# Optimization experiments

Measured on AMD Instinct MI355X. Metric: run time of the kernel, lower is better.

Reference implementation:

```python
import jax, jax.numpy as jnp
import numpy as np

NEG_SLOPE = 0.01  # torch nn.LeakyReLU default


def setup_inputs() -> dict:
    key = jax.random.key(0)
    k1, k2, k3 = jax.random.split(key, 3)
    B, H, D, L = 4, 8, 64, 2048
    q = jax.random.normal(k1, (B, H, D, L), dtype=jnp.float32)
    k = jax.random.normal(k2, (B, H, D, L), dtype=jnp.float32)
    v = jax.random.normal(k3, (B, H, D, L), dtype=jnp.float32)
    return {"q": q, "k": k, "v": v}


def reference(q, k, v):
    # q, k, v: [B, H, D, L] (note: feature dim BEFORE length, as in the torch module)
    d_tensor = q.shape[2]
    scale = 1.0 / np.sqrt(d_tensor).astype(np.float32)
    # scores = LeakyReLU(q^T k / sqrt(d)) : [B, H, Lq, Lk]
    scores = jnp.einsum('bhdq,bhdk->bhqk', q, k) * scale
    scores = jax.nn.leaky_relu(scores, negative_slope=NEG_SLOPE)
    psi = jax.nn.softmax(scores, axis=-1)
    # out = (psi @ v^T)^T : [B, H, D, Lq]
    out = jnp.einsum('bhqk,bhdk->bhdq', psi, v)
    return out
```

## Files before the change

kernel.cpp:

```cpp
#include <hip/hip_runtime.h>
#include <math.h>

#define DD 64
#define LL 2048
#define TQ 128
#define TK 64
#define NTHREADS 512
#define QSCALE 0.18033688011112042f

typedef __bf16 bf16_t;
typedef __bf16 bf16x8 __attribute__((ext_vector_type(8)));
typedef float f32x16 __attribute__((ext_vector_type(16)));

struct __align__(16) SMemA {
  bf16_t Qs[TQ][72];
  bf16_t Ks[TK][72];
  bf16_t Vs[DD][72];
};
union __align__(16) SMemU {
  SMemA a;
  float Oe[TQ][65];
};

__global__ __launch_bounds__(NTHREADS, 4)
void attn_flash_bf16(const float* __restrict__ q, const float* __restrict__ k,
                     const float* __restrict__ v, float* __restrict__ out) {
  __shared__ SMemU sm;
  __shared__ float rs1[TQ];
  const int tid  = threadIdx.x;
  const int w    = tid >> 6;
  const int lane = tid & 63;
  const int l31  = lane & 31;
  const int hh   = lane >> 5;
  const int strip = w & 3;
  const int half  = w >> 2;
  const int wbase = strip * 32;
  const int lkh   = half * 32;
  const int head = blockIdx.y;
  const int q0   = blockIdx.x * TQ;
  const size_t hoff = (size_t)head * DD * LL;
  const float* qp = q + hoff;
  const float* kp = k + hoff;
  const float* vp = v + hoff;

  {
    int lq  = tid & 127;
    int d0q = (tid >> 7) * 16;
    const float* src = qp + q0 + lq;
    for (int g = 0; g < 2; ++g) {
      bf16x8 pk;
      for (int j = 0; j < 8; ++j)
        pk[j] = (bf16_t)(src[(size_t)(d0q + g * 8 + j) * LL] * QSCALE);
      *(bf16x8*)&sm.a.Qs[lq][d0q + g * 8] = pk;
    }
  }

  const int klk = tid & 63;
  const int kd0 = (tid >> 6) * 8;
  const int vd  = tid >> 3;
  const int vc8 = (tid & 7) * 8;

  float  kreg[8];
  float4 vreg[2];
  {
    const float* ks = kp + klk;
    for (int j = 0; j < 8; ++j) kreg[j] = ks[(size_t)(kd0 + j) * LL];
    vreg[0] = *(const float4*)(vp + (size_t)vd * LL + vc8);
    vreg[1] = *(const float4*)(vp + (size_t)vd * LL + vc8 + 4);
  }

  __syncthreads();
  bf16x8 bq[4];
  for (int kk = 0; kk < 4; ++kk)
    bq[kk] = *(const bf16x8*)&sm.a.Qs[wbase + l31][kk * 16 + 8 * hh];

  f32x16 oacc[2];
  for (int dt = 0; dt < 2; ++dt)
    for (int r = 0; r < 16; ++r) oacc[dt][r] = 0.f;
  float rsum = 0.f;

  for (int t = 0; t < LL / TK; ++t) {
    __syncthreads();
    {
      bf16x8 pk;
      for (int j = 0; j < 8; ++j) pk[j] = (bf16_t)kreg[j];
      *(bf16x8*)&sm.a.Ks[klk][kd0] = pk;
      bf16x8 pv;
      pv[0] = (bf16_t)vreg[0].x; pv[1] = (bf16_t)vreg[0].y;
      pv[2] = (bf16_t)vreg[0].z; pv[3] = (bf16_t)vreg[0].w;
      pv[4] = (bf16_t)vreg[1].x; pv[5] = (bf16_t)vreg[1].y;
      pv[6] = (bf16_t)vreg[1].z; pv[7] = (bf16_t)vreg[1].w;
      *(bf16x8*)&sm.a.Vs[vd][vc8] = pv;
    }
    __syncthreads();

    if (t + 1 < LL / TK) {
      const int lk0n = (t + 1) * TK;
      const float* ks = kp + lk0n + klk;
      for (int j = 0; j < 8; ++j) kreg[j] = ks[(size_t)(kd0 + j) * LL];
      vreg[0] = *(const float4*)(vp + (size_t)vd * LL + lk0n + vc8);
      vreg[1] = *(const float4*)(vp + (size_t)vd * LL + lk0n + vc8 + 4);
    }

    f32x16 st;
    for (int r = 0; r < 16; ++r) st[r] = 0.f;
    for (int kk = 0; kk < 4; ++kk) {
      bf16x8 ak = *(const bf16x8*)&sm.a.Ks[lkh + l31][kk * 16 + 8 * hh];
      st = __builtin_amdgcn_mfma_f32_32x32x16_bf16(ak, bq[kk], st, 0, 0, 0);
    }

    unsigned pb[8];
    for (int r = 0; r < 16; ++r) {
      float s = st[r];
      s = fmaxf(s, 0.01f * s);
      float p = __builtin_amdgcn_exp2f(s);
      rsum += p;
      st[r] = p;
    }
    for (int qq = 0; qq < 8; ++qq) {
      union { bf16_t b[2]; unsigned u; } pk;
      pk.b[0] = (bf16_t)st[2 * qq];
      pk.b[1] = (bf16_t)st[2 * qq + 1];
      pb[qq] = pk.u;
    }

    for (int kk2 = 0; kk2 < 2; ++kk2) {
      unsigned l0 = pb[4 * kk2 + 0], l1 = pb[4 * kk2 + 1];
      unsigned l2 = pb[4 * kk2 + 2], l3 = pb[4 * kk2 + 3];
      unsigned s0 = hh ? l0 : l2;
      unsigned s1 = hh ? l1 : l3;
      unsigned f0 = (unsigned)__shfl_xor((int)s0, 32);
      unsigned f1 = (unsigned)__shfl_xor((int)s1, 32);
      union { unsigned u[4]; bf16x8 v; } ap;
      ap.u[0] = hh ? f0 : l0;
      ap.u[1] = hh ? f1 : l1;
      ap.u[2] = hh ? l2 : f0;
      ap.u[3] = hh ? l3 : f1;
      const int lkb = lkh + kk2 * 16 + 8 * hh;
      for (int dt = 0; dt < 2; ++dt) {
        bf16x8 bv = *(const bf16x8*)&sm.a.Vs[dt * 32 + l31][lkb];
        oacc[dt] = __builtin_amdgcn_mfma_f32_32x32x16_bf16(ap.v, bv, oacc[dt], 0, 0, 0);
      }
    }
  }

  float rtot = rsum + __shfl_xor(rsum, 32);
  __syncthreads();
  if (half == 1) {
    rs1[wbase + l31] = rtot;
    for (int r = 0; r < 16; ++r) {
      int row = (r & 3) + 8 * (r >> 2) + 4 * hh;
      for (int dt = 0; dt < 2; ++dt)
        sm.Oe[wbase + row][dt * 32 + l31] = oacc[dt][r];
    }
  }
  __syncthreads();
  if (half == 0) {
    float tot = rtot + rs1[wbase + l31];
    rs1[wbase + l31] = 1.0f / tot;
    float inv[16];
    for (int r = 0; r < 16; ++r) {
      int row = (r & 3) + 8 * (r >> 2) + 4 * hh;
      inv[r] = rs1[wbase + row];
    }
    for (int r = 0; r < 16; ++r) {
      int row = (r & 3) + 8 * (r >> 2) + 4 * hh;
      for (int dt = 0; dt < 2; ++dt) {
        int col = dt * 32 + l31;
        sm.Oe[wbase + row][col] = (oacc[dt][r] + sm.Oe[wbase + row][col]) * inv[r];
      }
    }
  }
  __syncthreads();
  float* op = out + hoff + q0;
  for (int i = 0; i < 16; ++i) {
    int idx = tid + NTHREADS * i;
    int d   = idx >> 7;
    int lq  = idx & 127;
    op[(size_t)d * LL + lq] = sm.Oe[lq][d];
  }
}

extern "C" void kernel_launch(void* const* d_in, const int* in_sizes, int n_in,
                              void* d_out, int out_size, void* d_ws, size_t ws_size,
                              hipStream_t stream) {
  const float* q = (const float*)d_in[0];
  const float* k = (const float*)d_in[1];
  const float* v = (const float*)d_in[2];
  float* out = (float*)d_out;
  dim3 grid(LL / TQ, 32);
  attn_flash_bf16<<<grid, NTHREADS, 0, stream>>>(q, k, v, out);
}
```

Baseline: 145.7 us.

## Double block threads to 1024, widen K tile to 128, drop register prefetch

Doubles the workgroup to 16 waves. Each strip of 32 query rows is now split four ways across the key dimension, with a key tile of 128, and the epilogue reduces four partial outputs through two shared buffers. The register-staged prefetch of the next K/V tile is removed, so global loads now happen directly before the barrier. Q fragments are reloaded from LDS inside the loop instead of being held in registers, trading register pressure for extra LDS reads. The launch bound of 1024 threads with 8 blocks per CU is a hint the hardware cannot meet, and occupancy is likely limited by registers and LDS.

```diff
diff --git a/kernel.cpp b/kernel.cpp
--- a/kernel.cpp
+++ b/kernel.cpp
@@ -4,8 +4,9 @@
 #define DD 64
 #define LL 2048
 #define TQ 128
-#define TK 64
-#define NTHREADS 512
+#define TK 128
+#define NTILES (LL / TK)
+#define NTHREADS 1024
 #define QSCALE 0.18033688011112042f
 
 typedef __bf16 bf16_t;
@@ -15,27 +16,28 @@
 struct __align__(16) SMemA {
   bf16_t Qs[TQ][72];
   bf16_t Ks[TK][72];
-  bf16_t Vs[DD][72];
+  bf16_t Vs[DD][136];
 };
-union __align__(16) SMemU {
-  SMemA a;
-  float Oe[TQ][65];
+struct __align__(16) SMemE {
+  float Oe1[TQ][65];
+  float Oe2[TQ][65];
 };
+union __align__(16) SMemU { SMemA a; SMemE e; };
 
-__global__ __launch_bounds__(NTHREADS, 4)
+__global__ __launch_bounds__(NTHREADS, 8)
 void attn_flash_bf16(const float* __restrict__ q, const float* __restrict__ k,
                      const float* __restrict__ v, float* __restrict__ out) {
   __shared__ SMemU sm;
-  __shared__ float rs1[TQ];
+  __shared__ float rsA[TQ], rsB[TQ];
   const int tid  = threadIdx.x;
   const int w    = tid >> 6;
   const int lane = tid & 63;
   const int l31  = lane & 31;
   const int hh   = lane >> 5;
   const int strip = w & 3;
-  const int half  = w >> 2;
+  const int quart = w >> 2;
   const int wbase = strip * 32;
-  const int lkh   = half * 32;
+  const int lkh   = quart * 32;
   const int head = blockIdx.y;
   const int q0   = blockIdx.x * TQ;
   const size_t hoff = (size_t)head * DD * LL;
@@ -44,69 +46,54 @@
   const float* vp = v + hoff;
 
   {
-    int lq  = tid & 127;
-    int d0q = (tid >> 7) * 16;
+    int lq = tid & 127;
+    int d0 = (tid >> 7) * 8;
     const float* src = qp + q0 + lq;
-    for (int g = 0; g < 2; ++g) {
-      bf16x8 pk;
-      for (int j = 0; j < 8; ++j)
-        pk[j] = (bf16_t)(src[(size_t)(d0q + g * 8 + j) * LL] * QSCALE);
-      *(bf16x8*)&sm.a.Qs[lq][d0q + g * 8] = pk;
-    }
+    bf16x8 pk;
+    for (int j = 0; j < 8; ++j)
+      pk[j] = (bf16_t)(src[(size_t)(d0 + j) * LL] * QSCALE);
+    *(bf16x8*)&sm.a.Qs[lq][d0] = pk;
   }
 
-  const int klk = tid & 63;
-  const int kd0 = (tid >> 6) * 8;
-  const int vd  = tid >> 3;
-  const int vc8 = (tid & 7) * 8;
-
-  float  kreg[8];
-  float4 vreg[2];
-  {
-    const float* ks = kp + klk;
-    for (int j = 0; j < 8; ++j) kreg[j] = ks[(size_t)(kd0 + j) * LL];
-    vreg[0] = *(const float4*)(vp + (size_t)vd * LL + vc8);
-    vreg[1] = *(const float4*)(vp + (size_t)vd * LL + vc8 + 4);
-  }
-
-  __syncthreads();
-  bf16x8 bq[4];
-  for (int kk = 0; kk < 4; ++kk)
-    bq[kk] = *(const bf16x8*)&sm.a.Qs[wbase + l31][kk * 16 + 8 * hh];
+  const int klk = tid & 127;
+  const int kd0 = (tid >> 7) * 8;
+  const int vd  = tid >> 4;
+  const int vc8 = (tid & 15) * 8;
 
   f32x16 oacc[2];
   for (int dt = 0; dt < 2; ++dt)
     for (int r = 0; r < 16; ++r) oacc[dt][r] = 0.f;
   float rsum = 0.f;
 
-  for (int t = 0; t < LL / TK; ++t) {
+  for (int t = 0; t < NTILES; ++t) {
+    const int lk0 = t * TK;
     __syncthreads();
     {
+      const float* src = kp + lk0 + klk;
       bf16x8 pk;
-      for (int j = 0; j < 8; ++j) pk[j] = (bf16_t)kreg[j];
+      for (int j = 0; j < 8; ++j)
+        pk[j] = (bf16_t)src[(size_t)(kd0 + j) * LL];
       *(bf16x8*)&sm.a.Ks[klk][kd0] = pk;
+    }
+    {
+      const float* src = vp + (size_t)vd * LL + lk0 + vc8;
+      float4 a0 = *(const float4*)src;
+      float4 a1 = *(const float4*)(src + 4);
       bf16x8 pv;
-      pv[0] = (bf16_t)vreg[0].x; pv[1] = (bf16_t)vreg[0].y;
-      pv[2] = (bf16_t)vreg[0].z; pv[3] = (bf16_t)vreg[0].w;
-      pv[4] = (bf16_t)vreg[1].x; pv[5] = (bf16_t)vreg[1].y;
-      pv[6] = (bf16_t)vreg[1].z; pv[7] = (bf16_t)vreg[1].w;
+      pv[0] = (bf16_t)a0.x; pv[1] = (bf16_t)a0.y;
+      pv[2] = (bf16_t)a0.z; pv[3] = (bf16_t)a0.w;
+      pv[4] = (bf16_t)a1.x; pv[5] = (bf16_t)a1.y;
+      pv[6] = (bf16_t)a1.z; pv[7] = (bf16_t)a1.w;
       *(bf16x8*)&sm.a.Vs[vd][vc8] = pv;
     }
     __syncthreads();
-
-    if (t + 1 < LL / TK) {
-      const int lk0n = (t + 1) * TK;
-      const float* ks = kp + lk0n + klk;
-      for (int j = 0; j < 8; ++j) kreg[j] = ks[(size_t)(kd0 + j) * LL];
-      vreg[0] = *(const float4*)(vp + (size_t)vd * LL + lk0n + vc8);
-      vreg[1] = *(const float4*)(vp + (size_t)vd * LL + lk0n + vc8 + 4);
-    }
 
     f32x16 st;
     for (int r = 0; r < 16; ++r) st[r] = 0.f;
     for (int kk = 0; kk < 4; ++kk) {
       bf16x8 ak = *(const bf16x8*)&sm.a.Ks[lkh + l31][kk * 16 + 8 * hh];
-      st = __builtin_amdgcn_mfma_f32_32x32x16_bf16(ak, bq[kk], st, 0, 0, 0);
+      bf16x8 bq = *(const bf16x8*)&sm.a.Qs[wbase + l31][kk * 16 + 8 * hh];
+      st = __builtin_amdgcn_mfma_f32_32x32x16_bf16(ak, bq, st, 0, 0, 0);
     }
 
     unsigned pb[8];
@@ -146,38 +133,46 @@
 
   float rtot = rsum + __shfl_xor(rsum, 32);
   __syncthreads();
-  if (half == 1) {
-    rs1[wbase + l31] = rtot;
+  if (quart == 0) {
+    rsA[wbase + l31] = rtot;
     for (int r = 0; r < 16; ++r) {
       int row = (r & 3) + 8 * (r >> 2) + 4 * hh;
       for (int dt = 0; dt < 2; ++dt)
-        sm.Oe[wbase + row][dt * 32 + l31] = oacc[dt][r];
+        sm.e.Oe1[wbase + row][dt * 32 + l31] = oacc[dt][r];
+    }
+  } else if (quart == 2) {
+    rsB[wbase + l31] = rtot;
+    for (int r = 0; r < 16; ++r) {
+      int row = (r & 3) + 8 * (r >> 2) + 4 * hh;
+      for (int dt = 0; dt < 2; ++dt)
+        sm.e.Oe2[wbase + row][dt * 32 + l31] = oacc[dt][r];
     }
   }
   __syncthreads();
-  if (half == 0) {
-    float tot = rtot + rs1[wbase + l31];
-    rs1[wbase + l31] = 1.0f / tot;
-    float inv[16];
+  if (quart == 1) {
+    rsA[wbase + l31] += rtot;
     for (int r = 0; r < 16; ++r) {
       int row = (r & 3) + 8 * (r >> 2) + 4 * hh;
-      inv[r] = rs1[wbase + row];
+      for (int dt = 0; dt < 2; ++dt)
+        sm.e.Oe1[wbase + row][dt * 32 + l31] += oacc[dt][r];
     }
+  } else if (quart == 3) {
+    rsB[wbase + l31] += rtot;
     for (int r = 0; r < 16; ++r) {
       int row = (r & 3) + 8 * (r >> 2) + 4 * hh;
-      for (int dt = 0; dt < 2; ++dt) {
-        int col = dt * 32 + l31;
-        sm.Oe[wbase + row][col] = (oacc[dt][r] + sm.Oe[wbase + row][col]) * inv[r];
-      }
+      for (int dt = 0; dt < 2; ++dt)
+        sm.e.Oe2[wbase + row][dt * 32 + l31] += oacc[dt][r];
     }
   }
   __syncthreads();
+  if (tid < TQ) rsA[tid] = 1.0f / (rsA[tid] + rsB[tid]);
+  __syncthreads();
   float* op = out + hoff + q0;
-  for (int i = 0; i < 16; ++i) {
+  for (int i = 0; i < 8; ++i) {
     int idx = tid + NTHREADS * i;
     int d   = idx >> 7;
     int lq  = idx & 127;
-    op[(size_t)d * LL + lq] = sm.Oe[lq][d];
+    op[(size_t)d * LL + lq] = (sm.e.Oe1[lq][d] + sm.e.Oe2[lq][d]) * rsA[lq];
   }
 }
 
```

Measured after the change: 506.0 us. 3.47x slower.

## Pre-convert Q/K/V to bf16 (transposed Q/K) in workspace before attention

Applied to the files above, without the earlier changes.

Adds pre-pass kernels that convert Q and K to bf16 and transpose them to [L, D] layout, with the softmax scale folded into Q, and convert V to bf16 in place. The attention kernel then reads half as many bytes per K/V tile, with contiguous 16-byte loads instead of strided scalar float loads, and no longer converts inside the inner loop. K and V are each re-read by 16 query blocks, so this lowers repeated global traffic. In exchange it adds three extra launches and a full write/read of the bf16 copies. The old kernel is kept as a fallback when the workspace is too small.

```diff
diff --git a/kernel.cpp b/kernel.cpp
--- a/kernel.cpp
+++ b/kernel.cpp
@@ -5,7 +5,9 @@
 #define LL 2048
 #define TQ 128
 #define TK 64
+#define NTILES (LL / TK)
 #define NTHREADS 512
+#define NHEADS 32
 #define QSCALE 0.18033688011112042f
 
 typedef __bf16 bf16_t;
@@ -22,9 +24,190 @@
   float Oe[TQ][65];
 };
 
+__global__ __launch_bounds__(256)
+void prep_t(const float* __restrict__ src, bf16_t* __restrict__ dst, float scale) {
+  __shared__ bf16_t tile[64][72];
+  const int tid  = threadIdx.x;
+  const int head = blockIdx.y;
+  const int l0   = blockIdx.x * 64;
+  const float* sp = src + (size_t)head * DD * LL;
+  {
+    int d  = tid >> 2;
+    int lg = (tid & 3) * 16;
+    const float* rp = sp + (size_t)d * LL + l0 + lg;
+    for (int g = 0; g < 4; ++g) {
+      float4 a = *(const float4*)(rp + 4 * g);
+      tile[lg + 4 * g + 0][d] = (bf16_t)(a.x * scale);
+      tile[lg + 4 * g + 1][d] = (bf16_t)(a.y * scale);
+      tile[lg + 4 * g + 2][d] = (bf16_t)(a.z * scale);
+      tile[lg + 4 * g + 3][d] = (bf16_t)(a.w * scale);
+    }
+  }
+  __syncthreads();
+  {
+    int l  = tid & 63;
+    int dh = (tid >> 6) * 16;
+    bf16x8 r0 = *(const bf16x8*)&tile[l][dh];
+    bf16x8 r1 = *(const bf16x8*)&tile[l][dh + 8];
+    bf16_t* op = dst + ((size_t)head * LL + l0 + l) * DD + dh;
+    *(bf16x8*)op = r0;
+    *(bf16x8*)(op + 8) = r1;
+  }
+}
+
+__global__ __launch_bounds__(256)
+void prep_c(const float* __restrict__ src, bf16_t* __restrict__ dst) {
+  size_t i = ((size_t)blockIdx.x * 256 + threadIdx.x) * 8;
+  float4 a = *(const float4*)(src + i);
+  float4 b = *(const float4*)(src + i + 4);
+  bf16x8 p;
+  p[0] = (bf16_t)a.x; p[1] = (bf16_t)a.y; p[2] = (bf16_t)a.z; p[3] = (bf16_t)a.w;
+  p[4] = (bf16_t)b.x; p[5] = (bf16_t)b.y; p[6] = (bf16_t)b.z; p[7] = (bf16_t)b.w;
+  *(bf16x8*)(dst + i) = p;
+}
+
 __global__ __launch_bounds__(NTHREADS, 4)
-void attn_flash_bf16(const float* __restrict__ q, const float* __restrict__ k,
-                     const float* __restrict__ v, float* __restrict__ out) {
+void attn_flash_bf16(const bf16_t* __restrict__ Qt, const bf16_t* __restrict__ Kt,
+                     const bf16_t* __restrict__ Vb, float* __restrict__ out) {
+  __shared__ SMemU sm;
+  __shared__ float rs1[TQ];
+  const int tid  = threadIdx.x;
+  const int w    = tid >> 6;
+  const int lane = tid & 63;
+  const int l31  = lane & 31;
+  const int hh   = lane >> 5;
+  const int strip = w & 3;
+  const int half  = w >> 2;
+  const int wbase = strip * 32;
+  const int lkh   = half * 32;
+  const int head = blockIdx.y;
+  const int q0   = blockIdx.x * TQ;
+  const bf16_t* qp = Qt + (size_t)head * LL * DD;
+  const bf16_t* kp = Kt + (size_t)head * LL * DD;
+  const bf16_t* vp = Vb + (size_t)head * DD * LL;
+
+  {
+    int lq  = tid & 127;
+    int d0q = (tid >> 7) * 16;
+    const bf16_t* src = qp + (size_t)(q0 + lq) * DD + d0q;
+    bf16x8 a0 = *(const bf16x8*)src;
+    bf16x8 a1 = *(const bf16x8*)(src + 8);
+    *(bf16x8*)&sm.a.Qs[lq][d0q] = a0;
+    *(bf16x8*)&sm.a.Qs[lq][d0q + 8] = a1;
+  }
+
+  const int klk = tid & 63;
+  const int kd0 = (tid >> 6) * 8;
+  const int vd  = tid >> 3;
+  const int vc8 = (tid & 7) * 8;
+
+  bf16x8 kreg = *(const bf16x8*)(kp + (size_t)klk * DD + kd0);
+  bf16x8 vreg = *(const bf16x8*)(vp + (size_t)vd * LL + vc8);
+
+  __syncthreads();
+  bf16x8 bq[4];
+  for (int kk = 0; kk < 4; ++kk)
+    bq[kk] = *(const bf16x8*)&sm.a.Qs[wbase + l31][kk * 16 + 8 * hh];
+
+  f32x16 oacc[2];
+  for (int dt = 0; dt < 2; ++dt)
+    for (int r = 0; r < 16; ++r) oacc[dt][r] = 0.f;
+  float rsum = 0.f;
+
+  for (int t = 0; t < NTILES; ++t) {
+    __syncthreads();
+    *(bf16x8*)&sm.a.Ks[klk][kd0] = kreg;
+    *(bf16x8*)&sm.a.Vs[vd][vc8]  = vreg;
+    __syncthreads();
+
+    if (t + 1 < NTILES) {
+      const int lk0n = (t + 1) * TK;
+      kreg = *(const bf16x8*)(kp + (size_t)(lk0n + klk) * DD + kd0);
+      vreg = *(const bf16x8*)(vp + (size_t)vd * LL + lk0n + vc8);
+    }
+
+    f32x16 st;
+    for (int r = 0; r < 16; ++r) st[r] = 0.f;
+    for (int kk = 0; kk < 4; ++kk) {
+      bf16x8 ak = *(const bf16x8*)&sm.a.Ks[lkh + l31][kk * 16 + 8 * hh];
+      st = __builtin_amdgcn_mfma_f32_32x32x16_bf16(ak, bq[kk], st, 0, 0, 0);
+    }
+
+    unsigned pb[8];
+    for (int r = 0; r < 16; ++r) {
+      float s = st[r];
+      s = fmaxf(s, 0.01f * s);
+      float p = __builtin_amdgcn_exp2f(s);
+      rsum += p;
+      st[r] = p;
+    }
+    for (int qq = 0; qq < 8; ++qq) {
+      union { bf16_t b[2]; unsigned u; } pk;
+      pk.b[0] = (bf16_t)st[2 * qq];
+      pk.b[1] = (bf16_t)st[2 * qq + 1];
+      pb[qq] = pk.u;
+    }
+
+    for (int kk2 = 0; kk2 < 2; ++kk2) {
+      unsigned l0 = pb[4 * kk2 + 0], l1 = pb[4 * kk2 + 1];
+      unsigned l2 = pb[4 * kk2 + 2], l3 = pb[4 * kk2 + 3];
+      unsigned s0 = hh ? l0 : l2;
+      unsigned s1 = hh ? l1 : l3;
+      unsigned f0 = (unsigned)__shfl_xor((int)s0, 32);
+      unsigned f1 = (unsigned)__shfl_xor((int)s1, 32);
+      union { unsigned u[4]; bf16x8 v; } ap;
+      ap.u[0] = hh ? f0 : l0;
+      ap.u[1] = hh ? f1 : l1;
+      ap.u[2] = hh ? l2 : f0;
+      ap.u[3] = hh ? l3 : f1;
+      const int lkb = lkh + kk2 * 16 + 8 * hh;
+      for (int dt = 0; dt < 2; ++dt) {
+        bf16x8 bv = *(const bf16x8*)&sm.a.Vs[dt * 32 + l31][lkb];
+        oacc[dt] = __builtin_amdgcn_mfma_f32_32x32x16_bf16(ap.v, bv, oacc[dt], 0, 0, 0);
+      }
+    }
+  }
+
+  float rtot = rsum + __shfl_xor(rsum, 32);
+  __syncthreads();
+  if (half == 1) {
+    rs1[wbase + l31] = rtot;
+    for (int r = 0; r < 16; ++r) {
+      int row = (r & 3) + 8 * (r >> 2) + 4 * hh;
+      for (int dt = 0; dt < 2; ++dt)
+        sm.Oe[wbase + row][dt * 32 + l31] = oacc[dt][r];
+    }
+  }
+  __syncthreads();
+  if (half == 0) {
+    float tot = rtot + rs1[wbase + l31];
+    rs1[wbase + l31] = 1.0f / tot;
+    float inv[16];
+    for (int r = 0; r < 16; ++r) {
+      int row = (r & 3) + 8 * (r >> 2) + 4 * hh;
+      inv[r] = rs1[wbase + row];
+    }
+    for (int r = 0; r < 16; ++r) {
+      int row = (r & 3) + 8 * (r >> 2) + 4 * hh;
+      for (int dt = 0; dt < 2; ++dt) {
+        int col = dt * 32 + l31;
+        sm.Oe[wbase + row][col] = (oacc[dt][r] + sm.Oe[wbase + row][col]) * inv[r];
+      }
+    }
+  }
+  __syncthreads();
+  float* op = out + (size_t)head * DD * LL + q0;
+  for (int i = 0; i < 16; ++i) {
+    int idx = tid + NTHREADS * i;
+    int d   = idx >> 7;
+    int lq  = idx & 127;
+    op[(size_t)d * LL + lq] = sm.Oe[lq][d];
+  }
+}
+
+__global__ __launch_bounds__(NTHREADS, 4)
+void attn_flash_fb(const float* __restrict__ q, const float* __restrict__ k,
+                   const float* __restrict__ v, float* __restrict__ out) {
   __shared__ SMemU sm;
   __shared__ float rs1[TQ];
   const int tid  = threadIdx.x;
@@ -42,7 +225,6 @@
   const float* qp = q + hoff;
   const float* kp = k + hoff;
   const float* vp = v + hoff;
-
   {
     int lq  = tid & 127;
     int d0q = (tid >> 7) * 16;
@@ -54,12 +236,10 @@
       *(bf16x8*)&sm.a.Qs[lq][d0q + g * 8] = pk;
     }
   }
-
   const int klk = tid & 63;
   const int kd0 = (tid >> 6) * 8;
   const int vd  = tid >> 3;
   const int vc8 = (tid & 7) * 8;
-
   float  kreg[8];
   float4 vreg[2];
   {
@@ -68,18 +248,15 @@
     vreg[0] = *(const float4*)(vp + (size_t)vd * LL + vc8);
     vreg[1] = *(const float4*)(vp + (size_t)vd * LL + vc8 + 4);
   }
-
   __syncthreads();
   bf16x8 bq[4];
   for (int kk = 0; kk < 4; ++kk)
     bq[kk] = *(const bf16x8*)&sm.a.Qs[wbase + l31][kk * 16 + 8 * hh];
-
   f32x16 oacc[2];
   for (int dt = 0; dt < 2; ++dt)
     for (int r = 0; r < 16; ++r) oacc[dt][r] = 0.f;
   float rsum = 0.f;
-
-  for (int t = 0; t < LL / TK; ++t) {
+  for (int t = 0; t < NTILES; ++t) {
     __syncthreads();
     {
       bf16x8 pk;
@@ -93,22 +270,19 @@
       *(bf16x8*)&sm.a.Vs[vd][vc8] = pv;
     }
     __syncthreads();
-
-    if (t + 1 < LL / TK) {
+    if (t + 1 < NTILES) {
       const int lk0n = (t + 1) * TK;
       const float* ks = kp + lk0n + klk;
       for (int j = 0; j < 8; ++j) kreg[j] = ks[(size_t)(kd0 + j) * LL];
       vreg[0] = *(const float4*)(vp + (size_t)vd * LL + lk0n + vc8);
       vreg[1] = *(const float4*)(vp + (size_t)vd * LL + lk0n + vc8 + 4);
     }
-
     f32x16 st;
     for (int r = 0; r < 16; ++r) st[r] = 0.f;
     for (int kk = 0; kk < 4; ++kk) {
       bf16x8 ak = *(const bf16x8*)&sm.a.Ks[lkh + l31][kk * 16 + 8 * hh];
       st = __builtin_amdgcn_mfma_f32_32x32x16_bf16(ak, bq[kk], st, 0, 0, 0);
     }
-
     unsigned pb[8];
     for (int r = 0; r < 16; ++r) {
       float s = st[r];
@@ -123,7 +297,6 @@
       pk.b[1] = (bf16_t)st[2 * qq + 1];
       pb[qq] = pk.u;
     }
-
     for (int kk2 = 0; kk2 < 2; ++kk2) {
       unsigned l0 = pb[4 * kk2 + 0], l1 = pb[4 * kk2 + 1];
       unsigned l2 = pb[4 * kk2 + 2], l3 = pb[4 * kk2 + 3];
@@ -143,7 +316,6 @@
       }
     }
   }
-
   float rtot = rsum + __shfl_xor(rsum, 32);
   __syncthreads();
   if (half == 1) {
@@ -188,6 +360,19 @@
   const float* k = (const float*)d_in[1];
   const float* v = (const float*)d_in[2];
   float* out = (float*)d_out;
-  dim3 grid(LL / TQ, 32);
-  attn_flash_bf16<<<grid, NTHREADS, 0, stream>>>(q, k, v, out);
-}
+  const size_t tsz = (size_t)NHEADS * LL * DD;
+  const size_t need = 3 * tsz * sizeof(bf16_t);
+  dim3 grid(LL / TQ, NHEADS);
+  if (ws_size >= need) {
+    bf16_t* Qt = (bf16_t*)d_ws;
+    bf16_t* Kt = Qt + tsz;
+    bf16_t* Vb = Kt + tsz;
+    dim3 pg(LL / 64, NHEADS);
+    prep_t<<<pg, 256, 0, stream>>>(q, Qt, QSCALE);
+    prep_t<<<pg, 256, 0, stream>>>(k, Kt, 1.0f);
+    prep_c<<<(unsigned)(tsz / (256 * 8)), 256, 0, stream>>>(v, Vb);
+    attn_flash_bf16<<<grid, NTHREADS, 0, stream>>>(Qt, Kt, Vb, out);
+  } else {
+    attn_flash_fb<<<grid, NTHREADS, 0, stream>>>(q, k, v, out);
+  }
+}
```

After: 155.4 us. +6.6%, slower.
